# Kernel tuning notes

Hardware: AMD Instinct MI355X
Metric: run time of the kernel (lower is better)

Reference implementation:

```python
import jax, jax.numpy as jnp
import numpy as np

B, NQ, NK = 4, 2048, 2048
D_MODEL, D_K, D_V, H = 1024, 1024, 1024, 16


def setup_inputs() -> dict:
    key = jax.random.key(0)
    ks = jax.random.split(key, 8)
    return {
        "queries": jax.random.normal(ks[0], (B, NQ, D_MODEL), dtype=jnp.float32),
        "keys": jax.random.normal(ks[1], (B, NK, D_MODEL), dtype=jnp.float32),
        "values": jax.random.normal(ks[2], (B, NK, D_MODEL), dtype=jnp.float32),
        # nn.Linear weights init.normal_(std=0.001); stored here in (in, out) layout
        "Wq": jax.random.normal(ks[3], (D_MODEL, D_K), dtype=jnp.float32) * 0.001,
        "Wk": jax.random.normal(ks[4], (D_MODEL, D_K), dtype=jnp.float32) * 0.001,
        "Wv": jax.random.normal(ks[5], (D_MODEL, D_V), dtype=jnp.float32) * 0.001,
        "Wo": jax.random.normal(ks[6], (D_V, D_MODEL), dtype=jnp.float32) * 0.001,
        "bo": jnp.zeros((D_MODEL,), dtype=jnp.float32),
    }


def reference(queries, keys, values, Wq, Wk, Wv, Wo, bo):
    b_s, nq, _ = queries.shape
    nk = keys.shape[1]
    hd_k = D_K // H  # per-head key dim
    hd_v = D_V // H  # per-head value dim
    # projections -> [b, h, n, hd]
    q = (queries @ Wq).reshape(b_s, nq, H, hd_k).transpose(0, 2, 1, 3)
    k = (keys @ Wk).reshape(b_s, nk, H, hd_k).transpose(0, 2, 1, 3)
    v = (values @ Wv).reshape(b_s, nk, H, hd_v).transpose(0, 2, 1, 3)
    # NOTE: original scales by sqrt(d_k) (full d_k), not per-head dim
    att = jnp.einsum("bhqd,bhkd->bhqk", q, k) / np.float32(np.sqrt(D_K))
    att = jax.nn.softmax(att, axis=-1)
    # dropout = identity (eval mode)
    out = jnp.einsum("bhqk,bhkd->bhqd", att, v)
    out = out.transpose(0, 2, 1, 3).reshape(b_s, nq, D_V)
    return out @ Wo + bo
```

## Files before the change

### kernel.cpp

```cpp
#include <hip/hip_runtime.h>


#define DM    1024
#define NSEQ  2048
#define HEADS 16
#define HD    64

typedef float floatx4 __attribute__((ext_vector_type(4)));
typedef short s16x4   __attribute__((ext_vector_type(4)));
typedef short s16x8   __attribute__((ext_vector_type(8)));
typedef unsigned int u32x4 __attribute__((ext_vector_type(4)));

static __device__ __forceinline__ floatx4 mfma_bf16(s16x8 a, s16x8 b, floatx4 c) {
  return __builtin_amdgcn_mfma_f32_16x16x32_bf16(a, b, c, 0, 0, 0);
}

static __device__ __forceinline__ void gload_lds16(const void* g, void* l) {
  __builtin_amdgcn_global_load_lds(
      (const __attribute__((address_space(1))) unsigned*)g,
      (__attribute__((address_space(3))) unsigned*)l, 16, 0, 0);
}

static __device__ __forceinline__ unsigned lds_addr(const void* p) {
  return (unsigned)(unsigned long long)p;
}

static __device__ __forceinline__ s16x8 ds_read_b128a(unsigned byteaddr) {
  s16x8 r;
  asm volatile("ds_read_b128 %0, %1" : "=v"(r) : "v"(byteaddr));
  return r;
}

#define SCHED0() __builtin_amdgcn_sched_barrier(0)
#define WAIT_LGKM0() \
  { asm volatile("s_waitcnt lgkmcnt(0)" ::: "memory"); __builtin_amdgcn_sched_barrier(0); }
#define WAIT_VMCNT(N) \
  { asm volatile("s_waitcnt vmcnt(" #N ")" ::: "memory"); __builtin_amdgcn_sched_barrier(0); }

static __device__ __forceinline__ short f2bf(float f) {
  unsigned u = __builtin_bit_cast(unsigned, f);
  u += 0x7FFFu + ((u >> 16) & 1u);
  return (short)(u >> 16);
}

static __device__ __forceinline__ unsigned cvtpk_bf16(float lo, float hi) {
  unsigned r;
  asm("v_cvt_pk_bf16_f32 %0, %1, %2" : "=v"(r) : "v"(lo), "v"(hi));
  return r;
}

static __device__ __forceinline__ unsigned pack2_bf16(float a, float b) {
  unsigned ua = __builtin_bit_cast(unsigned, a) + 0x8000u;
  unsigned ub = __builtin_bit_cast(unsigned, b) + 0x8000u;
#if __has_builtin(__builtin_amdgcn_perm)
  return __builtin_amdgcn_perm(ub, ua, 0x07060302u);
#else
  return (ub & 0xffff0000u) | (ua >> 16);
#endif
}

__global__ __launch_bounds__(256) void make_wgroups(
    const float* __restrict__ W0, const float* __restrict__ W1,
    const float* __restrict__ W2, const float* __restrict__ W3,
    short* __restrict__ G0, short* __restrict__ G1,
    short* __restrict__ G2, short* __restrict__ G3) {
  __shared__ float tile[64][68];
  const int m = blockIdx.z;
  const float* W = m == 0 ? W0 : m == 1 ? W1 : m == 2 ? W2 : W3;
  short*       G = m == 0 ? G0 : m == 1 ? G1 : m == 2 ? G2 : G3;
  const int nt = blockIdx.x, kt = blockIdx.y;
  const int n0 = nt * 64, k0 = kt * 64;
  const int t = threadIdx.x;
  for (int j = 0; j < 4; j++) {
    int idx = j * 256 + t, r = idx >> 4, cq = idx & 15;
    *(floatx4*)&tile[r][cq * 4] = *(const floatx4*)(W + (long)(k0 + r) * DM + n0 + cq * 4);
  }
  __syncthreads();
  for (int j = 0; j < 2; j++) {
    int ci = j * 256 + t;
    int lm = ci & 15, quad = (ci >> 4) & 3, kk = (ci >> 6) & 1, gl = ci >> 7;
    s16x8 v;
#pragma unroll
    for (int e = 0; e < 8; e++) v[e] = f2bf(tile[kk * 32 + quad * 8 + e][gl * 16 + lm]);
    long addr;
    if (m < 3) {
      int ct = nt >> 2, g16 = (nt & 3) * 4 + gl;
      addr = ((long)(ct * 16 + kt)) * 16384 + (g16 * 2 + kk) * 512 + (quad * 16 + lm) * 8;
    } else {
      int ct = nt >> 1, g16 = (nt & 1) * 4 + gl;
      addr = ((long)(ct * 16 + kt)) * 8192 + (g16 * 2 + kk) * 512 + (quad * 16 + lm) * 8;
    }
    *(s16x8*)(G + addr) = v;
  }
}

__global__ __launch_bounds__(512, 2) void proj_kernel(
    const float* __restrict__ Aq, const float* __restrict__ Ak, const float* __restrict__ Av,
    const short* __restrict__ BgQ, const short* __restrict__ BgK, const short* __restrict__ BgV,
    short* __restrict__ Qh, short* __restrict__ KVg) {
  __shared__ short lds[3 * 24576];
  const int z = blockIdx.z;
  const float* A  = z == 0 ? Aq  : z == 1 ? Ak  : Av;
  const short* Bg = z == 0 ? BgQ : z == 1 ? BgK : BgV;
  const int t = threadIdx.x;
  const int w = t >> 6, l = t & 63, quad = l >> 4, lm = l & 15;
  const int wm = w >> 2, wn = w & 3;
  const int row0 = blockIdx.x * 128;
  const int ct = blockIdx.y;
  const int col0 = ct * 256;

  floatx4 acc[4][4];
  for (int mi = 0; mi < 4; mi++)
    for (int ni = 0; ni < 4; ni++) acc[mi][ni] = (floatx4){0.f, 0.f, 0.f, 0.f};

  floatx4 ar[2][2];
  auto loadA = [&](int ks) __attribute__((always_inline)) {
#pragma unroll
    for (int j = 0; j < 2; j++) {
      int tt = j * 512 + t, r = tt >> 3, c8 = (tt & 7) * 8;
      const float* p = A + (long)(row0 + r) * DM + ks * 64 + c8;
      ar[j][0] = *(const floatx4*)p;
      ar[j][1] = *(const floatx4*)(p + 4);
    }
  };
  auto writeA = [&](int buf) __attribute__((always_inline)) {
#pragma unroll
    for (int j = 0; j < 2; j++) {
      int tt = j * 512 + t, r = tt >> 3;
      int kk = (tt & 7) >> 2, q4 = tt & 3, lm2 = r & 15, g16 = r >> 4;
      u32x4 pk = {cvtpk_bf16(ar[j][0][0], ar[j][0][1]), cvtpk_bf16(ar[j][0][2], ar[j][0][3]),
                  cvtpk_bf16(ar[j][1][0], ar[j][1][1]), cvtpk_bf16(ar[j][1][2], ar[j][1][3])};
      int l3 = q4 * 16 + (lm2 ^ (q4 * 2));
      *(s16x8*)(lds + buf * 24576 + (g16 * 2 + kk) * 512 + l3 * 8) =
          __builtin_bit_cast(s16x8, pk);
    }
  };
  auto stageB = [&](int ks, int buf) __attribute__((always_inline)) {
    const long pan = ((long)(ct * 16 + ks)) * 16384;
#pragma unroll
    for (int i = 0; i < 4; i++) {
      int gb = w * 4 + i;
      const short* src = Bg + pan + gb * 512 + l * 8;
      gload_lds16(src, lds + buf * 24576 + 8192 + gb * 512);
    }
  };

  const unsigned lds0 = lds_addr(lds);
  auto process = [&](int buf) __attribute__((always_inline)) {
    const unsigned lbase = lds0 + buf * 49152u;
    const unsigned aswz = (quad * 16 + (lm ^ (quad * 2))) * 16;
#pragma unroll
    for (int kk = 0; kk < 2; kk++) {
      s16x8 af[4], bfr[4];
#pragma unroll
      for (int mi = 0; mi < 4; mi++)
        af[mi] = ds_read_b128a(lbase + ((wm * 4 + mi) * 2 + kk) * 1024 + aswz);
#pragma unroll
      for (int ni = 0; ni < 4; ni++)
        bfr[ni] = ds_read_b128a(lbase + 16384 + ((wn * 4 + ni) * 2 + kk) * 1024 + l * 16);
      WAIT_LGKM0();
      __builtin_amdgcn_s_setprio(1);
#pragma unroll
      for (int mi = 0; mi < 4; mi++)
#pragma unroll
        for (int ni = 0; ni < 4; ni++)
          acc[mi][ni] = mfma_bf16(af[mi], bfr[ni], acc[mi][ni]);
      __builtin_amdgcn_s_setprio(0);
    }
  };

  loadA(0);
  stageB(0, 0);
  stageB(1, 1);
  writeA(0);
  WAIT_VMCNT(4);
  WAIT_LGKM0();
  __builtin_amdgcn_s_barrier();

  for (int ks = 0; ks < 16; ++ks) {
    if (ks + 1 < 16) loadA(ks + 1);
    if (ks + 2 < 16) stageB(ks + 2, (ks + 2) % 3);
    SCHED0();
    process(ks % 3);
    if (ks + 1 < 16) writeA((ks + 1) % 3);
    WAIT_VMCNT(4);
    WAIT_LGKM0();
    __builtin_amdgcn_s_barrier();
  }

  const int rowbase = row0 + wm * 64;
  const int colbase = col0 + wn * 64;
  const int b = rowbase >> 11;
  const int h = colbase >> 6;
  const int rloc = rowbase & 2047;
  if (z == 0) {
    const float osc = 0.0450842200277801f;
    long base = ((long)(b * HEADS + h)) * NSEQ * HD;
    for (int mi = 0; mi < 4; mi++)
      for (int r = 0; r < 4; r++) {
        int q = rloc + mi * 16 + quad * 4 + r;
        long rowoff = base + (long)q * HD + lm;
        for (int ni = 0; ni < 4; ni++)
          Qh[rowoff + ni * 16] = f2bf(acc[mi][ni][r] * osc);
      }
  } else if (z == 1) {
    long bhb = ((long)(b * HEADS + h)) * 262144;
    for (int mi = 0; mi < 4; mi++)
      for (int r = 0; r < 4; r++) {
        int q = rloc + mi * 16 + quad * 4 + r;
        int tile = q >> 7, s = (q >> 5) & 3, jj = (q >> 4) & 1, lmk = q & 15;
        for (int ni = 0; ni < 4; ni++) {
          int c = ni >> 1, quadk = (ni * 2 + (lm >> 3)) & 3, ek = lm & 7;
          long addr = bhb + (long)tile * 16384 + (s * 4 + jj * 2 + c) * 512 +
                      (quadk * 16 + lmk) * 8 + ek;
          KVg[addr] = f2bf(acc[mi][ni][r]);
        }
      }
  } else {
    long bhb = ((long)(b * HEADS + h)) * 262144;
    for (int mi = 0; mi < 4; mi++)
      for (int r = 0; r < 4; r++) {
        int kc = rloc + (mi >> 1) * 32 + quad * 8 + (mi & 1) * 4 + r;
        int tile = kc >> 7, s = (kc >> 5) & 3, ev = (mi & 1) * 4 + r;
        for (int ni = 0; ni < 4; ni++) {
          long addr = bhb + (long)tile * 16384 + (16 + s * 4 + ni) * 512 +
                      (quad * 16 + lm) * 8 + ev;
          KVg[addr] = f2bf(acc[mi][ni][r]);
        }
      }
  }
}

__global__ __launch_bounds__(256, 2) void attn_kernel(
    const short* __restrict__ Qh, const short* __restrict__ KVg,
    short* __restrict__ Obf) {
  __shared__ short lds[2 * 16384];
  const int t = threadIdx.x;
  const int w = t >> 6, l = t & 63, quad = l >> 4, lm = l & 15;
  const int bh = blockIdx.x;
  const int qtile = blockIdx.y * 128 + w * 32;
  const short* Qp  = Qh  + (long)bh * NSEQ * HD;
  const short* KVp = KVg + (long)bh * 262144;

  s16x8 aq[2][2];
#pragma unroll
  for (int qi = 0; qi < 2; qi++)
#pragma unroll
    for (int c = 0; c < 2; c++)
      aq[qi][c] = *(const s16x8*)(Qp + (long)(qtile + qi * 16 + lm) * HD + c * 32 + quad * 8);

  floatx4 acc[2][4];
  float lsum[2] = {0.f, 0.f};
#pragma unroll
  for (int qi = 0; qi < 2; qi++)
#pragma unroll
    for (int n = 0; n < 4; n++) acc[qi][n] = (floatx4){0.f, 0.f, 0.f, 0.f};

  auto stage = [&](int kt, int buf) __attribute__((always_inline)) {
    short* base = lds + buf * 16384;
    const short* tsrc = KVp + (long)(kt >> 7) * 16384;
#pragma unroll
    for (int i = 0; i < 8; i++) {
      int g = w * 8 + i;
      gload_lds16(tsrc + g * 512 + l * 8, base + g * 512);
    }
  };

  auto process = [&](const short* Lb, int s) __attribute__((always_inline)) {
    s16x8 bk[2][2];
#pragma unroll
    for (int j = 0; j < 2; j++)
#pragma unroll
      for (int c = 0; c < 2; c++)
        bk[j][c] = *(const s16x8*)(Lb + ((s * 4 + j * 2 + c) * 64 + l) * 8);
    s16x8 vraw[4];
#pragma unroll
    for (int n = 0; n < 4; n++)
      vraw[n] = *(const s16x8*)(Lb + ((16 + s * 4 + n) * 64 + l) * 8);
#pragma unroll
    for (int qi = 0; qi < 2; qi++) {
      floatx4 sT[2];
      sT[0] = (floatx4){0.f, 0.f, 0.f, 0.f};
      sT[1] = (floatx4){0.f, 0.f, 0.f, 0.f};
      __builtin_amdgcn_s_setprio(1);
#pragma unroll
      for (int c = 0; c < 2; c++) {
        sT[0] = mfma_bf16(bk[0][c], aq[qi][c], sT[0]);
        sT[1] = mfma_bf16(bk[1][c], aq[qi][c], sT[1]);
      }
      __builtin_amdgcn_s_setprio(0);
      float p0 = __builtin_amdgcn_exp2f(sT[0][0]);
      float p1 = __builtin_amdgcn_exp2f(sT[0][1]);
      float p2 = __builtin_amdgcn_exp2f(sT[0][2]);
      float p3 = __builtin_amdgcn_exp2f(sT[0][3]);
      float p4 = __builtin_amdgcn_exp2f(sT[1][0]);
      float p5 = __builtin_amdgcn_exp2f(sT[1][1]);
      float p6 = __builtin_amdgcn_exp2f(sT[1][2]);
      float p7 = __builtin_amdgcn_exp2f(sT[1][3]);
      lsum[qi] += ((p0 + p1) + (p2 + p3)) + ((p4 + p5) + (p6 + p7));
      u32x4 pw = {pack2_bf16(p0, p1), pack2_bf16(p2, p3),
                  pack2_bf16(p4, p5), pack2_bf16(p6, p7)};
      s16x8 pcat = __builtin_bit_cast(s16x8, pw);
      __builtin_amdgcn_s_setprio(1);
#pragma unroll
      for (int n = 0; n < 4; n++)
        acc[qi][n] = mfma_bf16(vraw[n], pcat, acc[qi][n]);
      __builtin_amdgcn_s_setprio(0);
    }
  };

  stage(0, 0);
  __syncthreads();
  int cur = 0;
  for (int kt = 0; kt < NSEQ; kt += 128) {
    if (kt + 128 < NSEQ) stage(kt + 128, cur ^ 1);
    const short* Lb = lds + cur * 16384;
    process(Lb, 0);
    process(Lb, 1);
    process(Lb, 2);
    process(Lb, 3);
    __syncthreads();
    cur ^= 1;
  }

  const int b = bh >> 4, h = bh & 15;
  short* Ow = lds + w * 1152;
  const int erow = l >> 2, ecg = l & 3;
#pragma unroll
  for (int qi = 0; qi < 2; qi++) {
    float ls = lsum[qi];
    ls += __shfl_xor(ls, 16);
    ls += __shfl_xor(ls, 32);
    float rl = 1.0f / ls;
#pragma unroll
    for (int n = 0; n < 4; n++)
#pragma unroll
      for (int r = 0; r < 4; r++)
        Ow[lm * 72 + n * 16 + quad * 4 + r] = f2bf(acc[qi][n][r] * rl);
    s16x8 o0 = *(const s16x8*)(Ow + erow * 72 + ecg * 16);
    s16x8 o1 = *(const s16x8*)(Ow + erow * 72 + ecg * 16 + 8);
    long gaddr = ((long)(b * NSEQ + qtile + qi * 16 + erow)) * DM + h * HD + ecg * 16;
    *(s16x8*)(Obf + gaddr) = o0;
    *(s16x8*)(Obf + gaddr + 8) = o1;
  }
}

__global__ __launch_bounds__(256, 2) void out_kernel(
    const short* __restrict__ Ab, const short* __restrict__ WoG,
    const float* __restrict__ bias, float* __restrict__ Out) {
  __shared__ short lds[3 * 8192];
  const int t = threadIdx.x;
  const int w = t >> 6, l = t & 63, quad = l >> 4, lm = l & 15;
  const int wm = w >> 1, wn = w & 1;
  const int row0 = blockIdx.x * 128;
  const int ct = blockIdx.y;
  const int col0 = ct * 128;

  floatx4 acc[4][4];
  for (int mi = 0; mi < 4; mi++)
    for (int ni = 0; ni < 4; ni++) acc[mi][ni] = (floatx4){0.f, 0.f, 0.f, 0.f};

  s16x8 ar[2];
  auto loadA = [&](int kt) __attribute__((always_inline)) {
#pragma unroll
    for (int j = 0; j < 2; j++) {
      int tt = j * 256 + t, r = tt >> 2, c = tt & 3;
      ar[j] = *(const s16x8*)(Ab + (long)(row0 + r) * DM + kt * 32 + c * 8);
    }
  };
  auto writeA = [&](int buf) __attribute__((always_inline)) {
#pragma unroll
    for (int j = 0; j < 2; j++) {
      int tt = j * 256 + t, r = tt >> 2, q4 = tt & 3;
      int lm2 = r & 15, g16 = r >> 4;
      int l3 = q4 * 16 + (lm2 ^ (q4 * 2));
      *(s16x8*)(lds + buf * 8192 + g16 * 512 + l3 * 8) = ar[j];
    }
  };
  auto stageB = [&](int kt, int buf) __attribute__((always_inline)) {
    const long pan = ((long)(ct * 16 + (kt >> 1))) * 8192;
    const int kk = kt & 1;
#pragma unroll
    for (int i = 0; i < 2; i++) {
      int gb = w * 2 + i;
      const short* src = WoG + pan + (gb * 2 + kk) * 512 + l * 8;
      gload_lds16(src, lds + buf * 8192 + 4096 + gb * 512);
    }
  };
  const unsigned lds0 = lds_addr(lds);
  auto process = [&](int buf) __attribute__((always_inline)) {
    const unsigned lbase = lds0 + buf * 16384;
    const unsigned aswz = (quad * 16 + (lm ^ (quad * 2))) * 16;
    s16x8 af[4], bfr[4];
#pragma unroll
    for (int mi = 0; mi < 4; mi++)
      af[mi] = ds_read_b128a(lbase + (wm * 4 + mi) * 1024 + aswz);
#pragma unroll
    for (int ni = 0; ni < 4; ni++)
      bfr[ni] = ds_read_b128a(lbase + 8192 + (wn * 4 + ni) * 1024 + l * 16);
    WAIT_LGKM0();
    __builtin_amdgcn_s_setprio(1);
#pragma unroll
    for (int mi = 0; mi < 4; mi++)
#pragma unroll
      for (int ni = 0; ni < 4; ni++)
        acc[mi][ni] = mfma_bf16(af[mi], bfr[ni], acc[mi][ni]);
    __builtin_amdgcn_s_setprio(0);
  };

  loadA(0);
  stageB(0, 0);
  stageB(1, 1);
  writeA(0);
  WAIT_VMCNT(2);
  WAIT_LGKM0();
  __builtin_amdgcn_s_barrier();

  for (int kt = 0; kt < 32; ++kt) {
    if (kt + 1 < 32) loadA(kt + 1);
    if (kt + 2 < 32) stageB(kt + 2, (kt + 2) % 3);
    SCHED0();
    process(kt % 3);
    if (kt + 1 < 32) writeA((kt + 1) % 3);
    WAIT_VMCNT(2);
    WAIT_LGKM0();
    __builtin_amdgcn_s_barrier();
  }

  const int rowbase = row0 + wm * 64;
  const int colbase = col0 + wn * 64;
  for (int mi = 0; mi < 4; mi++)
    for (int r = 0; r < 4; r++) {
      int gr = rowbase + mi * 16 + quad * 4 + r;
      for (int ni = 0; ni < 4; ni++) {
        int gc = colbase + ni * 16 + lm;
        Out[(long)gr * DM + gc] = acc[mi][ni][r] + bias[gc];
      }
    }
}

extern "C" void kernel_launch(void* const* d_in, const int* in_sizes, int n_in,
                              void* d_out, int out_size, void* d_ws, size_t ws_size,
                              hipStream_t stream) {
  (void)in_sizes; (void)n_in; (void)out_size; (void)ws_size;
  const float* queries = (const float*)d_in[0];
  const float* keys    = (const float*)d_in[1];
  const float* values  = (const float*)d_in[2];
  const float* Wq = (const float*)d_in[3];
  const float* Wk = (const float*)d_in[4];
  const float* Wv = (const float*)d_in[5];
  const float* Wo = (const float*)d_in[6];
  const float* bo = (const float*)d_in[7];
  float* out = (float*)d_out;

  char* ws = (char*)d_ws;
  const size_t MB = 1024 * 1024;
  short* WqG = (short*)(ws + 0 * MB);
  short* WkG = (short*)(ws + 2 * MB);
  short* WvG = (short*)(ws + 4 * MB);
  short* WoG = (short*)(ws + 6 * MB);
  short* Qh  = (short*)(ws + 8 * MB);
  short* KVg = (short*)(ws + 24 * MB);
  short* Obf = (short*)(ws + 56 * MB);

  make_wgroups<<<dim3(16, 16, 4), 256, 0, stream>>>(
      Wq, Wk, Wv, Wo, WqG, WkG, WvG, WoG);
  proj_kernel<<<dim3(64, 4, 3), 512, 0, stream>>>(
      queries, keys, values, WqG, WkG, WvG, Qh, KVg);
  attn_kernel<<<dim3(64, 16), 256, 0, stream>>>(Qh, KVg, Obf);
  out_kernel<<<dim3(64, 8), 256, 0, stream>>>(Obf, WoG, bo, out);
}
```

Before: 321.6 us.

## Retile projection GEMM to 64x512 blocks with K-step 32 and double buffering

The projection kernel moves from 128x256 output tiles with a K-step of 64 and a three-stage LDS pipeline to 64x512 tiles with a K-step of 32 and two buffers. Each wave now owns a 64x64 column slice that shares one A tile, and the weight pre-layout is reorganised to match. The aim is to read each fp32 activation row once for many more output columns and to reduce LDS usage. In exchange it does twice as many barrier iterations with less pipelining depth, and only half the threads load A.

```diff
diff --git a/kernel.cpp b/kernel.cpp
--- a/kernel.cpp
+++ b/kernel.cpp
@@ -84,8 +84,10 @@
     for (int e = 0; e < 8; e++) v[e] = f2bf(tile[kk * 32 + quad * 8 + e][gl * 16 + lm]);
     long addr;
     if (m < 3) {
-      int ct = nt >> 2, g16 = (nt & 3) * 4 + gl;
-      addr = ((long)(ct * 16 + kt)) * 16384 + (g16 * 2 + kk) * 512 + (quad * 16 + lm) * 8;
+      int ct2 = nt >> 3;
+      int p = ct2 * 32 + kt * 2 + kk;
+      int gb = (nt & 7) * 4 + gl;
+      addr = (long)p * 16384 + gb * 512 + (quad * 16 + lm) * 8;
     } else {
       int ct = nt >> 1, g16 = (nt & 1) * 4 + gl;
       addr = ((long)(ct * 16 + kt)) * 8192 + (g16 * 2 + kk) * 512 + (quad * 16 + lm) * 8;
@@ -98,98 +100,85 @@
     const float* __restrict__ Aq, const float* __restrict__ Ak, const float* __restrict__ Av,
     const short* __restrict__ BgQ, const short* __restrict__ BgK, const short* __restrict__ BgV,
     short* __restrict__ Qh, short* __restrict__ KVg) {
-  __shared__ short lds[3 * 24576];
+  __shared__ short lds[2 * 18432];
   const int z = blockIdx.z;
   const float* A  = z == 0 ? Aq  : z == 1 ? Ak  : Av;
   const short* Bg = z == 0 ? BgQ : z == 1 ? BgK : BgV;
   const int t = threadIdx.x;
   const int w = t >> 6, l = t & 63, quad = l >> 4, lm = l & 15;
-  const int wm = w >> 2, wn = w & 3;
-  const int row0 = blockIdx.x * 128;
-  const int ct = blockIdx.y;
-  const int col0 = ct * 256;
+  const int row0 = blockIdx.x * 64;
+  const int ct2 = blockIdx.y;
+  const int col0 = ct2 * 512;
 
   floatx4 acc[4][4];
   for (int mi = 0; mi < 4; mi++)
     for (int ni = 0; ni < 4; ni++) acc[mi][ni] = (floatx4){0.f, 0.f, 0.f, 0.f};
 
-  floatx4 ar[2][2];
+  floatx4 a0, a1;
   auto loadA = [&](int ks) __attribute__((always_inline)) {
-#pragma unroll
-    for (int j = 0; j < 2; j++) {
-      int tt = j * 512 + t, r = tt >> 3, c8 = (tt & 7) * 8;
-      const float* p = A + (long)(row0 + r) * DM + ks * 64 + c8;
-      ar[j][0] = *(const floatx4*)p;
-      ar[j][1] = *(const floatx4*)(p + 4);
+    if (t < 256) {
+      const float* p = A + (long)(row0 + (t >> 2)) * DM + ks * 32 + (t & 3) * 8;
+      a0 = *(const floatx4*)p;
+      a1 = *(const floatx4*)(p + 4);
     }
   };
   auto writeA = [&](int buf) __attribute__((always_inline)) {
-#pragma unroll
-    for (int j = 0; j < 2; j++) {
-      int tt = j * 512 + t, r = tt >> 3;
-      int kk = (tt & 7) >> 2, q4 = tt & 3, lm2 = r & 15, g16 = r >> 4;
-      u32x4 pk = {cvtpk_bf16(ar[j][0][0], ar[j][0][1]), cvtpk_bf16(ar[j][0][2], ar[j][0][3]),
-                  cvtpk_bf16(ar[j][1][0], ar[j][1][1]), cvtpk_bf16(ar[j][1][2], ar[j][1][3])};
-      int l3 = q4 * 16 + (lm2 ^ (q4 * 2));
-      *(s16x8*)(lds + buf * 24576 + (g16 * 2 + kk) * 512 + l3 * 8) =
+    if (t < 256) {
+      int row = t >> 2, q = t & 3, lm2 = row & 15, g16 = row >> 4;
+      u32x4 pk = {cvtpk_bf16(a0[0], a0[1]), cvtpk_bf16(a0[2], a0[3]),
+                  cvtpk_bf16(a1[0], a1[1]), cvtpk_bf16(a1[2], a1[3])};
+      int s = q * 16 + (lm2 ^ (q * 2));
+      *(s16x8*)(lds + buf * 18432 + g16 * 512 + s * 8) =
           __builtin_bit_cast(s16x8, pk);
     }
   };
   auto stageB = [&](int ks, int buf) __attribute__((always_inline)) {
-    const long pan = ((long)(ct * 16 + ks)) * 16384;
+    const long pan = (long)(ct2 * 32 + ks) * 16384;
 #pragma unroll
     for (int i = 0; i < 4; i++) {
       int gb = w * 4 + i;
       const short* src = Bg + pan + gb * 512 + l * 8;
-      gload_lds16(src, lds + buf * 24576 + 8192 + gb * 512);
+      gload_lds16(src, lds + buf * 18432 + 2048 + gb * 512);
     }
   };
 
   const unsigned lds0 = lds_addr(lds);
   auto process = [&](int buf) __attribute__((always_inline)) {
-    const unsigned lbase = lds0 + buf * 49152u;
+    const unsigned lbase = lds0 + buf * 36864u;
     const unsigned aswz = (quad * 16 + (lm ^ (quad * 2))) * 16;
-#pragma unroll
-    for (int kk = 0; kk < 2; kk++) {
-      s16x8 af[4], bfr[4];
-#pragma unroll
-      for (int mi = 0; mi < 4; mi++)
-        af[mi] = ds_read_b128a(lbase + ((wm * 4 + mi) * 2 + kk) * 1024 + aswz);
+    s16x8 af[4], bfr[4];
+#pragma unroll
+    for (int mi = 0; mi < 4; mi++)
+      af[mi] = ds_read_b128a(lbase + mi * 1024 + aswz);
+#pragma unroll
+    for (int ni = 0; ni < 4; ni++)
+      bfr[ni] = ds_read_b128a(lbase + 4096 + (w * 4 + ni) * 1024 + l * 16);
+    WAIT_LGKM0();
+    __builtin_amdgcn_s_setprio(1);
+#pragma unroll
+    for (int mi = 0; mi < 4; mi++)
 #pragma unroll
       for (int ni = 0; ni < 4; ni++)
-        bfr[ni] = ds_read_b128a(lbase + 16384 + ((wn * 4 + ni) * 2 + kk) * 1024 + l * 16);
-      WAIT_LGKM0();
-      __builtin_amdgcn_s_setprio(1);
-#pragma unroll
-      for (int mi = 0; mi < 4; mi++)
-#pragma unroll
-        for (int ni = 0; ni < 4; ni++)
-          acc[mi][ni] = mfma_bf16(af[mi], bfr[ni], acc[mi][ni]);
-      __builtin_amdgcn_s_setprio(0);
-    }
+        acc[mi][ni] = mfma_bf16(af[mi], bfr[ni], acc[mi][ni]);
+    __builtin_amdgcn_s_setprio(0);
   };
 
   loadA(0);
   stageB(0, 0);
-  stageB(1, 1);
   writeA(0);
-  WAIT_VMCNT(4);
-  WAIT_LGKM0();
-  __builtin_amdgcn_s_barrier();
-
-  for (int ks = 0; ks < 16; ++ks) {
-    if (ks + 1 < 16) loadA(ks + 1);
-    if (ks + 2 < 16) stageB(ks + 2, (ks + 2) % 3);
+  __syncthreads();
+  int cur = 0;
+  for (int ks = 0; ks < 32; ++ks) {
+    if (ks + 1 < 32) { loadA(ks + 1); stageB(ks + 1, cur ^ 1); }
     SCHED0();
-    process(ks % 3);
-    if (ks + 1 < 16) writeA((ks + 1) % 3);
-    WAIT_VMCNT(4);
-    WAIT_LGKM0();
-    __builtin_amdgcn_s_barrier();
-  }
-
-  const int rowbase = row0 + wm * 64;
-  const int colbase = col0 + wn * 64;
+    process(cur);
+    if (ks + 1 < 32) writeA(cur ^ 1);
+    __syncthreads();
+    cur ^= 1;
+  }
+
+  const int rowbase = row0;
+  const int colbase = col0 + w * 64;
   const int b = rowbase >> 11;
   const int h = colbase >> 6;
   const int rloc = rowbase & 2047;
@@ -465,7 +454,7 @@
 
   make_wgroups<<<dim3(16, 16, 4), 256, 0, stream>>>(
       Wq, Wk, Wv, Wo, WqG, WkG, WvG, WoG);
-  proj_kernel<<<dim3(64, 4, 3), 512, 0, stream>>>(
+  proj_kernel<<<dim3(128, 2, 3), 512, 0, stream>>>(
       queries, keys, values, WqG, WkG, WvG, Qh, KVg);
   attn_kernel<<<dim3(64, 16), 256, 0, stream>>>(Qh, KVg, Obf);
   out_kernel<<<dim3(64, 8), 256, 0, stream>>>(Obf, WoG, bo, out);
```

Result: slower. 333.2 us (+3.6%).
